# Kernel tuning notes

Measured on AMD Instinct MI355X. Metric: run time of the kernel, lower is better.

The kernel has to match this reference:

```python
import jax, jax.numpy as jnp
import numpy as np

TEMPERATURE = 1.0  # module default current_temperature
TOP_K = 2
NUM_EXPERTS = 64
EPS = 1e-10


def setup_inputs() -> dict:
    key = jax.random.key(0)
    k1, k2 = jax.random.split(key)
    x = jax.random.normal(k1, (4, 4096, 2048), dtype=jnp.float32)
    # nn.Linear(d_model, num_experts) weight has shape [num_experts, d_model]
    W_gate = jax.random.normal(k2, (NUM_EXPERTS, 2048), dtype=jnp.float32) * (1.0 / np.sqrt(2048))
    return {"x": x, "W_gate": W_gate}


def reference(x, W_gate):
    # Gate GEMM: [B,S,D] x [E,D] -> [B,S,E]
    logits = jnp.einsum("bsd,ed->bse", x, W_gate)
    scaled = logits / TEMPERATURE
    # Full distribution over experts (for load-balancing loss)
    router_probs = jax.nn.softmax(scaled, axis=-1)
    # Top-k selection over the expert dim, then renormalize via softmax
    top_k_logits, top_k_indices = jax.lax.top_k(scaled, TOP_K)  # [B,S,K]
    top_k_weights = jax.nn.softmax(top_k_logits, axis=-1)
    # Routing stats (no-grad in torch; plain values here)
    entropy = -jnp.sum(router_probs * jnp.log(router_probs + EPS), axis=-1)
    routing_entropy = entropy.mean()
    selection_confidence = top_k_weights[:, :, 0].mean()
    counts = jnp.zeros((NUM_EXPERTS,), dtype=x.dtype).at[top_k_indices.reshape(-1)].add(1.0)
    expert_utilization = counts / (counts.sum() + EPS)
    return (top_k_weights, top_k_indices, router_probs,
            routing_entropy, selection_confidence, expert_utilization)
```

## Files before the change

### kernel.cpp

```cpp
#include <hip/hip_runtime.h>
#include <math.h>

#define NTOK 16384
#define DIM 2048
#define NEXP 64
#define TB 16
#define KC 32
#define NSTAGE (DIM / KC)

#define OFF_W    0
#define OFF_I    32768
#define OFF_P    65536
#define OFF_ENT  1114112
#define OFF_CONF 1114113
#define OFF_UTIL 1114114

typedef short s16x8 __attribute__((ext_vector_type(8)));
typedef float f32x4 __attribute__((ext_vector_type(4)));

__device__ __forceinline__ unsigned short f2bf(float v) {
    unsigned u = __builtin_bit_cast(unsigned, v);
    u = u + 0x7FFFu + ((u >> 16) & 1u);
    return (unsigned short)(u >> 16);
}
__device__ __forceinline__ float bf2f(unsigned short b) {
    return __builtin_bit_cast(float, (unsigned)b << 16);
}

__global__ void router_init(float* __restrict__ out) {
    int tid = threadIdx.x;
    if (tid < 66) out[OFF_ENT + tid] = 0.0f;
}

__global__ void router_wsplit(const float* __restrict__ Wg, uint4* __restrict__ wsp) {
    const int c = blockIdx.x;
    const int t = threadIdx.x;
    const int nt = t >> 6, l = t & 63;
    const int e  = 16 * nt + (l & 15);
    const int k0 = 32 * c + 8 * (l >> 4);
    const float* src = Wg + (size_t)e * DIM + k0;
    float4 a = *(const float4*)src;
    float4 b = *(const float4*)(src + 4);
    float v[8] = {a.x, a.y, a.z, a.w, b.x, b.y, b.z, b.w};
    unsigned short H[8], M[8], L[8];
    #pragma unroll
    for (int j = 0; j < 8; ++j) {
        H[j] = f2bf(v[j]);  float r = v[j] - bf2f(H[j]);
        M[j] = f2bf(r);     r = r - bf2f(M[j]);
        L[j] = f2bf(r);
    }
    uint4 ph, pm, pl;
    ph.x = H[0] | ((unsigned)H[1] << 16); ph.y = H[2] | ((unsigned)H[3] << 16);
    ph.z = H[4] | ((unsigned)H[5] << 16); ph.w = H[6] | ((unsigned)H[7] << 16);
    pm.x = M[0] | ((unsigned)M[1] << 16); pm.y = M[2] | ((unsigned)M[3] << 16);
    pm.z = M[4] | ((unsigned)M[5] << 16); pm.w = M[6] | ((unsigned)M[7] << 16);
    pl.x = L[0] | ((unsigned)L[1] << 16); pl.y = L[2] | ((unsigned)L[3] << 16);
    pl.z = L[4] | ((unsigned)L[5] << 16); pl.w = L[6] | ((unsigned)L[7] << 16);
    const int idx = c * 256 + t;
    wsp[idx]         = ph;
    wsp[16384 + idx] = pm;
    wsp[32768 + idx] = pl;
}

#define LOADX(p_, c_) { xset##p_[0] = xq[8*(c_) + 2*qd]; xset##p_[1] = xq[8*(c_) + 2*qd + 1]; }
#define LOADW(p_, c_) { const int idx_ = (c_)*256 + wv*64 + l;  \
                        wset##p_[0] = wq[idx_];                 \
                        wset##p_[1] = wq[16384 + idx_];         \
                        wset##p_[2] = wq[32768 + idx_]; }

#define CONVX(p_) {                                                      \
    float xv[8];                                                         \
    xv[0]=xset##p_[0].x; xv[1]=xset##p_[0].y; xv[2]=xset##p_[0].z; xv[3]=xset##p_[0].w; \
    xv[4]=xset##p_[1].x; xv[5]=xset##p_[1].y; xv[6]=xset##p_[1].z; xv[7]=xset##p_[1].w; \
    _Pragma("unroll")                                                    \
    for (int j = 0; j < 8; ++j) {                                        \
        unsigned u_  = __builtin_bit_cast(unsigned, xv[j]);              \
        unsigned hb_ = u_ & 0xFFFF0000u;                                 \
        float    r_  = xv[j] - __builtin_bit_cast(float, hb_);           \
        unsigned mb_ = __builtin_bit_cast(unsigned, r_) & 0xFFFF0000u;   \
        float    r2_ = r_ - __builtin_bit_cast(float, mb_);              \
        unsigned lb_ = __builtin_bit_cast(unsigned, r2_);                \
        ah[j] = (short)(hb_ >> 16);                                      \
        am[j] = (short)(mb_ >> 16);                                      \
        al[j] = (short)(lb_ >> 16);                                      \
    } }

#define COMPUTE(p_) {                                                    \
    s16x8 bh_ = __builtin_bit_cast(s16x8, wset##p_[0]);                  \
    s16x8 bm_ = __builtin_bit_cast(s16x8, wset##p_[1]);                  \
    s16x8 bl_ = __builtin_bit_cast(s16x8, wset##p_[2]);                  \
    acc0 = __builtin_amdgcn_mfma_f32_16x16x32_bf16(ah, bh_, acc0, 0, 0, 0); \
    acc1 = __builtin_amdgcn_mfma_f32_16x16x32_bf16(am, bh_, acc1, 0, 0, 0); \
    acc0 = __builtin_amdgcn_mfma_f32_16x16x32_bf16(ah, bm_, acc0, 0, 0, 0); \
    acc1 = __builtin_amdgcn_mfma_f32_16x16x32_bf16(am, bm_, acc1, 0, 0, 0); \
    acc0 = __builtin_amdgcn_mfma_f32_16x16x32_bf16(ah, bl_, acc0, 0, 0, 0); \
    acc1 = __builtin_amdgcn_mfma_f32_16x16x32_bf16(al, bh_, acc1, 0, 0, 0); \
    }

__global__ __launch_bounds__(256, 4) void router_main(
    const float* __restrict__ x, const uint4* __restrict__ wq,
    float* __restrict__ out)
{
    __shared__ float lg[TB][NEXP + 1];
    __shared__ float m1s[TB], rss[TB];
    __shared__ float s_ent, s_conf, s_cnt[NEXP];

    const int tid = threadIdx.x;
    const int l   = tid & 63;
    const int wv  = __builtin_amdgcn_readfirstlane(tid >> 6);
    const int qd  = l >> 4;
    const int t0  = blockIdx.x * TB;

    if (tid == 0) { s_ent = 0.0f; s_conf = 0.0f; }
    if (tid < NEXP) s_cnt[tid] = 0.0f;

    const float4* xq = (const float4*)(x + (size_t)(t0 + (l & 15)) * DIM);

    f32x4 acc0 = (f32x4)(0.0f), acc1 = (f32x4)(0.0f);
    s16x8 ah, am, al;
    float4 xset0[2], xset1[2];
    uint4  wset0[3], wset1[3];

    LOADX(0, 0); LOADX(1, 1);
    LOADW(0, 0); LOADW(1, 1);

    for (int c = 0; c < NSTAGE; c += 2) {
        CONVX(0);
        if (c + 2 < NSTAGE) LOADX(0, c + 2);
        COMPUTE(0);
        if (c + 2 < NSTAGE) LOADW(0, c + 2);
        CONVX(1);
        if (c + 3 < NSTAGE) LOADX(1, c + 3);
        COMPUTE(1);
        if (c + 3 < NSTAGE) LOADW(1, c + 3);
    }

    #pragma unroll
    for (int r = 0; r < 4; ++r)
        lg[4 * qd + r][16 * wv + (l & 15)] = acc0[r] + acc1[r];
    __syncthreads();

    if (tid < TB) {
        const int t = tid;
        float m1 = -INFINITY, m2 = -INFINITY;
        int i1 = 0, i2 = 0;
        for (int e = 0; e < NEXP; ++e) {
            float lv = lg[t][e];
            if (lv > m1)      { m2 = m1; i2 = i1; m1 = lv; i1 = e; }
            else if (lv > m2) { m2 = lv; i2 = e; }
        }
        float ssum = 0.0f, tsum = 0.0f;
        for (int e = 0; e < NEXP; ++e) {
            float d = lg[t][e] - m1;
            float ex = __expf(d);
            ssum += ex;
            tsum += d * ex;
        }
        float rs = 1.0f / ssum;
        float H  = logf(ssum) - tsum * rs;
        float e2 = __expf(m2 - m1);
        float rn = 1.0f / (1.0f + e2);
        float w0 = rn, w1v = e2 * rn;
        m1s[t] = m1; rss[t] = rs;

        *(float2*)&out[OFF_W + 2 * (t0 + t)] = make_float2(w0, w1v);
        *(float2*)&out[OFF_I + 2 * (t0 + t)] = make_float2((float)i1, (float)i2);

        atomicAdd(&s_ent,  H);
        atomicAdd(&s_conf, w0);
        atomicAdd(&s_cnt[i1], 1.0f);
        atomicAdd(&s_cnt[i2], 1.0f);
    }
    __syncthreads();

    {
        int t  = tid >> 4;
        int qq = tid & 15;
        float m  = m1s[t];
        float rs = rss[t];
        float4 pr;
        pr.x = __expf(lg[t][4 * qq + 0] - m) * rs;
        pr.y = __expf(lg[t][4 * qq + 1] - m) * rs;
        pr.z = __expf(lg[t][4 * qq + 2] - m) * rs;
        pr.w = __expf(lg[t][4 * qq + 3] - m) * rs;
        *(float4*)&out[OFF_P + (size_t)(t0 + t) * NEXP + 4 * qq] = pr;
    }

    if (tid == 0) {
        atomicAdd(&out[OFF_ENT],  s_ent  * (1.0f / 16384.0f));
        atomicAdd(&out[OFF_CONF], s_conf * (1.0f / 16384.0f));
    }
    if (tid < NEXP)
        atomicAdd(&out[OFF_UTIL + tid], s_cnt[tid] * (1.0f / 32768.0f));
}

extern "C" void kernel_launch(void* const* d_in, const int* in_sizes, int n_in,
                              void* d_out, int out_size, void* d_ws, size_t ws_size,
                              hipStream_t stream) {
    const float* x  = (const float*)d_in[0];
    const float* Wg = (const float*)d_in[1];
    float* out = (float*)d_out;
    (void)in_sizes; (void)n_in; (void)out_size; (void)ws_size;

    router_init<<<dim3(1), dim3(128), 0, stream>>>(out);
    router_wsplit<<<dim3(NSTAGE), dim3(256), 0, stream>>>(Wg, (uint4*)d_ws);
    router_main<<<dim3(NTOK / TB), dim3(256), 0, stream>>>(x, (const uint4*)d_ws, out);
}
```

Measured before the change: 281.3 us.

## Stage x tiles through swizzled LDS with 32-token blocks and 2x2 wave tiling

Tokens per block double from 16 to 32, and the four waves are arranged as 2 token halves by 2 expert-pair halves, so each wave computes two 16x16 accumulators. x is loaded coalesced from global memory into an XOR-swizzled, double-buffered LDS tile, with a register prefetch two stages ahead, and is then read back per wave. Each weight fragment is now reused across 16 more tokens, and each x fragment across two expert tiles. The cost is a block-wide barrier every stage, more registers (launch bounds drop to 2 blocks per CU), and half as many blocks.

```diff
diff --git a/kernel.cpp b/kernel.cpp
--- a/kernel.cpp
+++ b/kernel.cpp
@@ -4,9 +4,8 @@
 #define NTOK 16384
 #define DIM 2048
 #define NEXP 64
-#define TB 16
-#define KC 32
-#define NSTAGE (DIM / KC)
+#define TB 32
+#define NSTAGE 64
 
 #define OFF_W    0
 #define OFF_I    32768
@@ -62,16 +61,15 @@
     wsp[32768 + idx] = pl;
 }
 
-#define LOADX(p_, c_) { xset##p_[0] = xq[8*(c_) + 2*qd]; xset##p_[1] = xq[8*(c_) + 2*qd + 1]; }
-#define LOADW(p_, c_) { const int idx_ = (c_)*256 + wv*64 + l;  \
-                        wset##p_[0] = wq[idx_];                 \
-                        wset##p_[1] = wq[16384 + idx_];         \
-                        wset##p_[2] = wq[32768 + idx_]; }
-
-#define CONVX(p_) {                                                      \
+#define LOADW(W_, c_) { const int b_ = (c_)*256 + np*128 + l;  \
+    W_[0] = wq[b_];          W_[1] = wq[b_ + 64];              \
+    W_[2] = wq[16384 + b_];  W_[3] = wq[16384 + b_ + 64];      \
+    W_[4] = wq[32768 + b_];  W_[5] = wq[32768 + b_ + 64]; }
+
+#define CONVA(a0_, a1_) {                                                \
     float xv[8];                                                         \
-    xv[0]=xset##p_[0].x; xv[1]=xset##p_[0].y; xv[2]=xset##p_[0].z; xv[3]=xset##p_[0].w; \
-    xv[4]=xset##p_[1].x; xv[5]=xset##p_[1].y; xv[6]=xset##p_[1].z; xv[7]=xset##p_[1].w; \
+    xv[0]=a0_.x; xv[1]=a0_.y; xv[2]=a0_.z; xv[3]=a0_.w;                  \
+    xv[4]=a1_.x; xv[5]=a1_.y; xv[6]=a1_.z; xv[7]=a1_.w;                  \
     _Pragma("unroll")                                                    \
     for (int j = 0; j < 8; ++j) {                                        \
         unsigned u_  = __builtin_bit_cast(unsigned, xv[j]);              \
@@ -85,59 +83,99 @@
         al[j] = (short)(lb_ >> 16);                                      \
     } }
 
-#define COMPUTE(p_) {                                                    \
-    s16x8 bh_ = __builtin_bit_cast(s16x8, wset##p_[0]);                  \
-    s16x8 bm_ = __builtin_bit_cast(s16x8, wset##p_[1]);                  \
-    s16x8 bl_ = __builtin_bit_cast(s16x8, wset##p_[2]);                  \
-    acc0 = __builtin_amdgcn_mfma_f32_16x16x32_bf16(ah, bh_, acc0, 0, 0, 0); \
-    acc1 = __builtin_amdgcn_mfma_f32_16x16x32_bf16(am, bh_, acc1, 0, 0, 0); \
-    acc0 = __builtin_amdgcn_mfma_f32_16x16x32_bf16(ah, bm_, acc0, 0, 0, 0); \
-    acc1 = __builtin_amdgcn_mfma_f32_16x16x32_bf16(am, bm_, acc1, 0, 0, 0); \
-    acc0 = __builtin_amdgcn_mfma_f32_16x16x32_bf16(ah, bl_, acc0, 0, 0, 0); \
-    acc1 = __builtin_amdgcn_mfma_f32_16x16x32_bf16(al, bh_, acc1, 0, 0, 0); \
-    }
-
-__global__ __launch_bounds__(256, 4) void router_main(
+#define COMPUTE(W_) {                                                    \
+    s16x8 b0h_ = __builtin_bit_cast(s16x8, W_[0]);                       \
+    s16x8 b1h_ = __builtin_bit_cast(s16x8, W_[1]);                       \
+    s16x8 b0m_ = __builtin_bit_cast(s16x8, W_[2]);                       \
+    s16x8 b1m_ = __builtin_bit_cast(s16x8, W_[3]);                       \
+    s16x8 b0l_ = __builtin_bit_cast(s16x8, W_[4]);                       \
+    s16x8 b1l_ = __builtin_bit_cast(s16x8, W_[5]);                       \
+    acc0 = __builtin_amdgcn_mfma_f32_16x16x32_bf16(ah, b0h_, acc0, 0, 0, 0); \
+    acc1 = __builtin_amdgcn_mfma_f32_16x16x32_bf16(ah, b1h_, acc1, 0, 0, 0); \
+    acc0 = __builtin_amdgcn_mfma_f32_16x16x32_bf16(am, b0h_, acc0, 0, 0, 0); \
+    acc1 = __builtin_amdgcn_mfma_f32_16x16x32_bf16(am, b1h_, acc1, 0, 0, 0); \
+    acc0 = __builtin_amdgcn_mfma_f32_16x16x32_bf16(ah, b0m_, acc0, 0, 0, 0); \
+    acc1 = __builtin_amdgcn_mfma_f32_16x16x32_bf16(ah, b1m_, acc1, 0, 0, 0); \
+    acc0 = __builtin_amdgcn_mfma_f32_16x16x32_bf16(am, b0m_, acc0, 0, 0, 0); \
+    acc1 = __builtin_amdgcn_mfma_f32_16x16x32_bf16(am, b1m_, acc1, 0, 0, 0); \
+    acc0 = __builtin_amdgcn_mfma_f32_16x16x32_bf16(ah, b0l_, acc0, 0, 0, 0); \
+    acc1 = __builtin_amdgcn_mfma_f32_16x16x32_bf16(ah, b1l_, acc1, 0, 0, 0); \
+    acc0 = __builtin_amdgcn_mfma_f32_16x16x32_bf16(al, b0h_, acc0, 0, 0, 0); \
+    acc1 = __builtin_amdgcn_mfma_f32_16x16x32_bf16(al, b1h_, acc1, 0, 0, 0); \
+    }
+
+#define READA(buf_, cc_) {                                               \
+    const int sl0_ = (2*qd)     ^ (tl & 7);                              \
+    const int sl1_ = (2*qd + 1) ^ (tl & 7);                              \
+    float4 a0_ = *(const float4*)&Xs[buf_][cc_][tl][4*sl0_];             \
+    float4 a1_ = *(const float4*)&Xs[buf_][cc_][tl][4*sl1_];             \
+    CONVA(a0_, a1_);                                                     \
+    }
+
+__global__ __launch_bounds__(256, 2) void router_main(
     const float* __restrict__ x, const uint4* __restrict__ wq,
     float* __restrict__ out)
 {
+    __shared__ __align__(16) float Xs[2][2][TB][32];
     __shared__ float lg[TB][NEXP + 1];
     __shared__ float m1s[TB], rss[TB];
     __shared__ float s_ent, s_conf, s_cnt[NEXP];
 
     const int tid = threadIdx.x;
     const int l   = tid & 63;
-    const int wv  = __builtin_amdgcn_readfirstlane(tid >> 6);
+    const int w   = tid >> 6;
+    const int np  = __builtin_amdgcn_readfirstlane(w >> 1);
+    const int tt  = w & 1;
     const int qd  = l >> 4;
+    const int tl  = tt * 16 + (l & 15);
     const int t0  = blockIdx.x * TB;
 
     if (tid == 0) { s_ent = 0.0f; s_conf = 0.0f; }
     if (tid < NEXP) s_cnt[tid] = 0.0f;
 
-    const float4* xq = (const float4*)(x + (size_t)(t0 + (l & 15)) * DIM);
+    const int st  = tid >> 3;
+    const int sq  = tid & 7;
+    const int gkq = sq ^ (st & 7);
+    const float* xsrc = x + (size_t)(t0 + st) * DIM + 4 * gkq;
 
     f32x4 acc0 = (f32x4)(0.0f), acc1 = (f32x4)(0.0f);
     s16x8 ah, am, al;
-    float4 xset0[2], xset1[2];
-    uint4  wset0[3], wset1[3];
-
-    LOADX(0, 0); LOADX(1, 1);
-    LOADW(0, 0); LOADW(1, 1);
-
-    for (int c = 0; c < NSTAGE; c += 2) {
-        CONVX(0);
-        if (c + 2 < NSTAGE) LOADX(0, c + 2);
-        COMPUTE(0);
-        if (c + 2 < NSTAGE) LOADW(0, c + 2);
-        CONVX(1);
-        if (c + 3 < NSTAGE) LOADX(1, c + 3);
-        COMPUTE(1);
-        if (c + 3 < NSTAGE) LOADW(1, c + 3);
+    uint4 wA[6], wB[6];
+    float4 xr0, xr1;
+
+    xr0 = *(const float4*)(xsrc);
+    xr1 = *(const float4*)(xsrc + 32);
+    LOADW(wA, 0); LOADW(wB, 1);
+    *(float4*)&Xs[0][0][st][4 * sq] = xr0;
+    *(float4*)&Xs[0][1][st][4 * sq] = xr1;
+    xr0 = *(const float4*)(xsrc + 64);
+    xr1 = *(const float4*)(xsrc + 96);
+    __syncthreads();
+
+    for (int s = 0; s < NSTAGE; s += 2) {
+        const int buf = (s >> 1) & 1;
+        if (s + 2 < NSTAGE) {
+            *(float4*)&Xs[buf ^ 1][0][st][4 * sq] = xr0;
+            *(float4*)&Xs[buf ^ 1][1][st][4 * sq] = xr1;
+        }
+        if (s + 4 < NSTAGE) {
+            xr0 = *(const float4*)(xsrc + (s + 4) * 32);
+            xr1 = *(const float4*)(xsrc + (s + 5) * 32);
+        }
+        READA(buf, 0);
+        COMPUTE(wA);
+        if (s + 2 < NSTAGE) LOADW(wA, s + 2);
+        READA(buf, 1);
+        COMPUTE(wB);
+        if (s + 3 < NSTAGE) LOADW(wB, s + 3);
+        __syncthreads();
     }
 
     #pragma unroll
-    for (int r = 0; r < 4; ++r)
-        lg[4 * qd + r][16 * wv + (l & 15)] = acc0[r] + acc1[r];
+    for (int r = 0; r < 4; ++r) {
+        lg[tt * 16 + 4 * qd + r][np * 32 + (l & 15)]      = acc0[r];
+        lg[tt * 16 + 4 * qd + r][np * 32 + 16 + (l & 15)] = acc1[r];
+    }
     __syncthreads();
 
     if (tid < TB) {
@@ -173,9 +211,11 @@
     }
     __syncthreads();
 
-    {
-        int t  = tid >> 4;
-        int qq = tid & 15;
+    #pragma unroll
+    for (int p = 0; p < 2; ++p) {
+        int Q  = tid + 256 * p;
+        int t  = Q >> 4;
+        int qq = Q & 15;
         float m  = m1s[t];
         float rs = rss[t];
         float4 pr;
```

Measured after the change: 240.3 us. -14.6%, faster.
